# Kernel optimization log

Hardware: AMD Instinct MI355X
Metric: run time of the kernel (lower is better)

The kernel has to match this reference:

```python
import jax, jax.numpy as jnp
import numpy as np

D_MODEL = 1024
N_HEADS = 16
D_HEAD = D_MODEL // N_HEADS


def setup_inputs() -> dict:
    key = jax.random.key(0)
    ks = jax.random.split(key, 6)
    B, LQ, LK = 4, 512, 4096
    scale = 1.0 / np.sqrt(D_MODEL)
    return {
        "q_in": jax.random.normal(ks[0], (B, LQ, D_MODEL), dtype=jnp.float32),
        "mem": jax.random.normal(ks[1], (B, LK, D_MODEL), dtype=jnp.float32),
        "mem_mask": jnp.ones((B, 1, 1, LK), dtype=bool),
        "Wq": jax.random.normal(ks[2], (D_MODEL, D_MODEL), dtype=jnp.float32) * scale,
        "Wk": jax.random.normal(ks[3], (D_MODEL, D_MODEL), dtype=jnp.float32) * scale,
        "Wv": jax.random.normal(ks[4], (D_MODEL, D_MODEL), dtype=jnp.float32) * scale,
        "Wo": jax.random.normal(ks[5], (D_MODEL, D_MODEL), dtype=jnp.float32) * scale,
    }


def _split_heads(x):
    B, L, D = x.shape
    return x.reshape(B, L, N_HEADS, D_HEAD).transpose(0, 2, 1, 3)  # [B,H,L,Dh]


def reference(q_in, mem, mem_mask, Wq, Wk, Wv, Wo):
    # Linear layers use y = x @ W.T (torch nn.Linear convention, bias=False)
    q = _split_heads(q_in @ Wq.T)   # [B,H,Lq,Dh]
    k = _split_heads(mem @ Wk.T)    # [B,H,Lk,Dh]
    v = _split_heads(mem @ Wv.T)    # [B,H,Lk,Dh]
    scores = jnp.einsum('bhqd,bhkd->bhqk', q, k) / jnp.sqrt(jnp.float32(D_HEAD))
    scores = jnp.where(mem_mask, scores, -jnp.inf)
    attn = jax.nn.softmax(scores, axis=-1)  # dropout is identity at eval
    out = jnp.einsum('bhqk,bhkd->bhqd', attn, v)  # [B,H,Lq,Dh]
    B, H, LQ, Dh = out.shape
    out = out.transpose(0, 2, 1, 3).reshape(B, LQ, H * Dh)
    return out @ Wo.T
```

## Files before the change

kernel.cpp:

```cpp
#include <hip/hip_runtime.h>

#define D_MODEL 1024
#define NH 16
#define DH 64
#define BB 4
#define LQ 512
#define LK 4096

typedef __attribute__((ext_vector_type(8))) short bf16x8;
typedef __attribute__((ext_vector_type(4))) short bf16x4;
typedef __attribute__((ext_vector_type(4))) float f32x4;
typedef __attribute__((ext_vector_type(4))) unsigned short us4;

union U4 { unsigned int u[2]; bf16x4 v; };
union U8 { unsigned int u[4]; bf16x8 v; };

#define MFMA32(a, b, c) __builtin_amdgcn_mfma_f32_16x16x32_bf16(a, b, c, 0, 0, 0)

#if __has_builtin(__builtin_amdgcn_mfma_f32_16x16x16bf16_1k)
#define HAVE_MFMA16 1
#define MFMA16(a, b, c) __builtin_amdgcn_mfma_f32_16x16x16bf16_1k(a, b, c, 0, 0, 0)
#else
#define HAVE_MFMA16 0
#endif

#if __has_builtin(__builtin_amdgcn_exp2f)
#define EXP2F __builtin_amdgcn_exp2f
#else
__device__ __forceinline__ float EXP2F(float x) { return __expf(x * 0.69314718056f); }
#endif

#define PIPE_BAR(KEEP) asm volatile("s_waitcnt vmcnt(" #KEEP ") lgkmcnt(0)\n\ts_barrier" ::: "memory")
#define END_BAR()      asm volatile("s_waitcnt lgkmcnt(0)\n\ts_barrier" ::: "memory")

__device__ __forceinline__ unsigned short f2bf(float f) {
    unsigned int u = __float_as_uint(f);
    u += 0x7fffu + ((u >> 16) & 1u);
    return (unsigned short)(u >> 16);
}
__device__ __forceinline__ unsigned int packrn(float a, float b) {
    unsigned int ua = __float_as_uint(a) + 0x8000u;
    unsigned int ub = __float_as_uint(b) + 0x8000u;
    return __builtin_amdgcn_perm(ub, ua, 0x07060302u);
}
__device__ __forceinline__ void gld16(const void* g, void* l) {
    __builtin_amdgcn_global_load_lds(
        (__attribute__((address_space(1))) void*)(g),
        (__attribute__((address_space(3))) void*)(l), 16, 0, 0);
}
__device__ __forceinline__ unsigned int bperm(int srclane4, unsigned int v) {
    return (unsigned int)__builtin_amdgcn_ds_bpermute(srclane4, (int)v);
}

__global__ __launch_bounds__(256) void cvt_all(const float* __restrict__ q,
                                               const float* __restrict__ mem,
                                               const float* __restrict__ w0, const float* __restrict__ w1,
                                               const float* __restrict__ w2, const float* __restrict__ w3,
                                               unsigned short* __restrict__ dst) {
    constexpr size_t EQ = (size_t)BB * LQ * D_MODEL;
    constexpr size_t EM = (size_t)BB * LK * D_MODEL;
    constexpr size_t EW = (size_t)D_MODEL * D_MODEL;
    constexpr size_t R1 = EQ + EM;
    size_t i = ((size_t)blockIdx.x * 256 + threadIdx.x) * 4;
    const float* s; size_t o;
    if (i < EQ)                { s = q;   o = i; }
    else if (i < R1)           { s = mem; o = i - EQ; }
    else if (i < R1 + EW)      { s = w0;  o = i - R1; }
    else if (i < R1 + 2 * EW)  { s = w1;  o = i - R1 - EW; }
    else if (i < R1 + 3 * EW)  { s = w2;  o = i - R1 - 2 * EW; }
    else                       { s = w3;  o = i - R1 - 3 * EW; }
    float4 v = *(const float4*)(s + o);
    us4 ob;
    ob.x = f2bf(v.x); ob.y = f2bf(v.y); ob.z = f2bf(v.z); ob.w = f2bf(v.w);
    *(us4*)(dst + i) = ob;
}

#define GEMM_DECLS                                                                 \
    const int tid = threadIdx.x;                                                   \
    const int w = tid >> 6, lane = tid & 63;                                       \
    const int wr = (w >> 1) * 64, wc = (w & 1) * 64;                               \
    const int srow = lane >> 3, ssw = ((lane & 7) ^ srow) * 8;                     \
    const int fr = lane & 15, g = lane >> 4, frx = fr & 7;                         \
    f32x4 zero = {0.f, 0.f, 0.f, 0.f};                                             \
    f32x4 acc[4][4];                                                               \
    for (int i = 0; i < 4; ++i)                                                    \
        for (int j = 0; j < 4; ++j) acc[i][j] = zero;                              \
    const unsigned short* ga = A + (size_t)(m0 + w * 32 + srow) * 1024 + ssw;      \
    const unsigned short* gb = Bw + (size_t)(n0 + w * 32 + srow) * 1024 + ssw;

#define GEMM_ISSUE(PAR) do {                                                       \
    unsigned short* da = As + (PAR) * (128 * 64) + (w * 32) * 64;                  \
    unsigned short* db = Bs + (PAR) * (128 * 64) + (w * 32) * 64;                  \
    for (int c = 0; c < 4; ++c) {                                                  \
        gld16(ga + (size_t)c * 8 * 1024, da + c * 8 * 64);                         \
        gld16(gb + (size_t)c * 8 * 1024, db + c * 8 * 64);                         \
    }                                                                              \
    ga += 64; gb += 64;                                                            \
} while (0)

#define GEMM_COMPUTE(PAR) do {                                                     \
    const unsigned short* Ap = As + (PAR) * (128 * 64);                            \
    const unsigned short* Bp = Bs + (PAR) * (128 * 64);                            \
    for (int ks = 0; ks < 2; ++ks) {                                               \
        const int fx = ((ks * 4 + g) ^ frx) * 8;                                   \
        bf16x8 af[4], bfr[4];                                                      \
        for (int i = 0; i < 4; ++i) af[i] = *(const bf16x8*)(Ap + (wr + 16 * i + fr) * 64 + fx); \
        for (int j = 0; j < 4; ++j) bfr[j] = *(const bf16x8*)(Bp + (wc + 16 * j + fr) * 64 + fx); \
        for (int i = 0; i < 4; ++i)                                                \
            for (int j = 0; j < 4; ++j)                                            \
                acc[i][j] = MFMA32(af[i], bfr[j], acc[i][j]);                      \
    }                                                                              \
} while (0)

#define GEMM_PIPELINE                                                              \
    GEMM_ISSUE(0); GEMM_ISSUE(1);                                                  \
    for (int it = 0; it < 14; ++it) {                                              \
        PIPE_BAR(8);                                                               \
        GEMM_COMPUTE(it & 1);                                                      \
        END_BAR();                                                                 \
        GEMM_ISSUE(it & 1);                                                        \
    }                                                                              \
    PIPE_BAR(8);                                                                   \
    GEMM_COMPUTE(0);                                                               \
    PIPE_BAR(0);                                                                   \
    GEMM_COMPUTE(1);

#define SLOT_SH 8192

#define STAGE2(GB, LB, S, H) do {                                                  \
    const unsigned short* gs_ = (GB) + (size_t)(H) * 32;                           \
    unsigned short* ld_ = (LB) + (S) * SLOT_SH + tid * 8;                          \
    gld16(gs_, ld_);                                                               \
    gld16(gs_ + (size_t)131072, ld_ + 4096);          \
} while (0)

#define RD_A8(DST, SLOT) do {                                                      \
    const unsigned short* Ap_ = As + (size_t)(SLOT) * SLOT_SH + aoff;              \
    _Pragma("unroll")                                                              \
    for (int ii_ = 0; ii_ < 8; ++ii_)                                              \
        DST[ii_] = *(const bf16x8*)(Ap_ + ii_ * 512);                              \
} while (0)

#define RD_B(DST, SLOT) do {                                                       \
    const unsigned short* Bp_ = Bs + (size_t)(SLOT) * SLOT_SH + boff;              \
    _Pragma("unroll")                                                              \
    for (int jj_ = 0; jj_ < 4; ++jj_)                                              \
        DST[jj_] = *(const bf16x8*)(Bp_ + jj_ * 512);                              \
} while (0)

#define MM32(AF, BF) do {                                                          \
    __builtin_amdgcn_s_setprio(1);                                                 \
    _Pragma("unroll")                                                              \
    for (int ii = 0; ii < 8; ++ii) {                                               \
        _Pragma("unroll")                                                          \
        for (int jj = 0; jj < 4; ++jj)                                             \
            acc[ii][jj] = MFMA32(AF[ii], BF[jj], acc[ii][jj]);                     \
    }                                                                              \
    __builtin_amdgcn_s_setprio(0);                                                 \
} while (0)

#define VW(N)  asm volatile("s_waitcnt vmcnt(" #N ")" ::: "memory")
#define PEND() asm volatile("s_waitcnt lgkmcnt(0)\n\ts_barrier" ::: "memory")

#define WIN(H, AFC, BFC, AFN, BFN) do {                                            \
    const int sn_ = ((H) + 1) & 3;                                                 \
    RD_A8(AFN, sn_); RD_B(BFN, sn_);                                               \
    STAGE2(gA, As, ((H) + 3) & 3, (H) + 3);                                        \
    STAGE2(gB, Bs, ((H) + 3) & 3, (H) + 3);                                        \
    MM32(AFC, BFC);                                                                \
    VW(4);                                                                         \
    PEND();                                                                        \
} while (0)

__global__ __launch_bounds__(512, 2) void proj256(const unsigned short* __restrict__ memb,
                                                  const unsigned short* __restrict__ W,
                                                  unsigned short* __restrict__ Kp,
                                                  unsigned short* __restrict__ Vt) {
    __shared__ alignas(16) unsigned short As[4 * SLOT_SH];
    __shared__ alignas(16) unsigned short Bs[4 * SLOT_SH];
    const int x = blockIdx.x;
    const int xcd = x & 7, s = x >> 3;
    const int rnd = s >> 5, i5 = s & 31;
    const int mt = xcd * 8 + rnd * 4 + (i5 >> 3);
    const int strip = i5 & 7;
    const int isV = strip >> 2, nt = strip & 3;
    const int m0 = mt * 256, n0 = nt * 256;
    const unsigned short* Bw = W + ((size_t)(1 + isV) << 20);

    const int tid = threadIdx.x;
    const int lane = tid & 63, wid = tid >> 6;
    const int wm = wid >> 2, wn = wid & 3;
    const int fr = lane & 15, g = lane >> 4;
    const int sfr = (fr >> 1) & 3;
    const int aoff = (wm * 128 + fr) * 32 + ((g ^ sfr) << 3);
    const int boff = (wn * 64 + fr) * 32 + ((g ^ sfr) << 3);

    f32x4 zero = {0.f, 0.f, 0.f, 0.f};
    f32x4 acc[8][4];
#pragma unroll
    for (int i = 0; i < 8; ++i)
#pragma unroll
        for (int j = 0; j < 4; ++j) acc[i][j] = zero;

    const int srow = tid >> 2;
    const int scg = (tid & 3) ^ ((tid >> 3) & 3);
    const unsigned short* gA = memb + (size_t)(m0 + srow) * 1024 + scg * 8;
    const unsigned short* gB = Bw + (size_t)(n0 + srow) * 1024 + scg * 8;

    bf16x8 afA[8], afB[8], bfA[4], bfB[4];

    STAGE2(gA, As, 0, 0); STAGE2(gB, Bs, 0, 0);
    STAGE2(gA, As, 1, 1); STAGE2(gB, Bs, 1, 1);
    STAGE2(gA, As, 2, 2); STAGE2(gB, Bs, 2, 2);
    VW(4);
    asm volatile("s_barrier" ::: "memory");
    RD_A8(afA, 0); RD_B(bfA, 0);

    for (int u = 0; u < 14; ++u) {
        WIN(2 * u,     afA, bfA, afB, bfB);
        WIN(2 * u + 1, afB, bfB, afA, bfA);
    }
    WIN(28, afA, bfA, afB, bfB);
    RD_A8(afA, 2); RD_B(bfA, 2);
    MM32(afB, bfB);
    VW(0);
    PEND();
    RD_A8(afB, 3); RD_B(bfB, 3);
    MM32(afA, bfA);
    PEND();
    MM32(afB, bfB);

    const int cl = fr;
    if (!isV) {
#pragma unroll
        for (int i = 0; i < 8; ++i)
#pragma unroll
            for (int j = 0; j < 4; ++j)
#pragma unroll
                for (int r = 0; r < 4; ++r) {
                    int m = m0 + wm * 128 + 16 * i + g * 4 + r;
                    int n = n0 + wn * 64 + 16 * j + cl;
                    Kp[(size_t)m * 1024 + n] = f2bf(acc[i][j][r]);
                }
    } else {
#pragma unroll
        for (int i = 0; i < 8; ++i)
#pragma unroll
            for (int j = 0; j < 4; ++j) {
                int m = m0 + wm * 128 + 16 * i + g * 4;
                int n = n0 + wn * 64 + 16 * j + cl;
                int b = m >> 12, tt2 = m & 4095;
                int h = n >> 6, d = n & 63;
                us4 ov;
                ov.x = f2bf(acc[i][j][0]); ov.y = f2bf(acc[i][j][1]);
                ov.z = f2bf(acc[i][j][2]); ov.w = f2bf(acc[i][j][3]);
                *(us4*)(Vt + ((size_t)(b * NH + h) * DH + d) * LK + tt2) = ov;
            }
    }
}

__global__ __launch_bounds__(256, 2) void proj_q(const unsigned short* __restrict__ qb,
                                                 const unsigned short* __restrict__ W,
                                                 unsigned short* __restrict__ Qp) {
    __shared__ alignas(16) unsigned short As[2 * 128 * 64];
    __shared__ alignas(16) unsigned short Bs[2 * 128 * 64];
    const int x = blockIdx.x;
    const int mt = x & 15, nt = x >> 4;
    const unsigned short* A = qb;
    const unsigned short* Bw = W;
    const int m0 = mt * 128, n0 = nt * 128;

    GEMM_DECLS
    GEMM_PIPELINE

    const int cl = lane & 15;
    const float QSCALE = 0.18033688011112042f;
    for (int i = 0; i < 4; ++i)
        for (int j = 0; j < 4; ++j)
            for (int r = 0; r < 4; ++r) {
                int m = m0 + wr + 16 * i + g * 4 + r;
                int n = n0 + wc + 16 * j + cl;
                Qp[(size_t)m * 1024 + n] = f2bf(acc[i][j][r] * QSCALE);
            }
}

__global__ __launch_bounds__(256, 2) void gemm_o(const unsigned short* __restrict__ A,
                                                 const unsigned short* __restrict__ Bw,
                                                 float* __restrict__ C) {
    __shared__ alignas(16) unsigned short As[2 * 128 * 64];
    __shared__ alignas(16) unsigned short Bs[2 * 128 * 64];
    const int m0 = blockIdx.x * 128, n0 = blockIdx.y * 128;

    GEMM_DECLS
    GEMM_PIPELINE

    const int cl = lane & 15;
    for (int i = 0; i < 4; ++i)
        for (int j = 0; j < 4; ++j)
            for (int r = 0; r < 4; ++r) {
                int m = m0 + wr + 16 * i + g * 4 + r;
                int n = n0 + wc + 16 * j + cl;
                C[(size_t)m * 1024 + n] = acc[i][j][r];
            }
}

__global__ __launch_bounds__(256, 4) void attn(const unsigned short* __restrict__ Qp,
                                               const unsigned short* __restrict__ Kp,
                                               const unsigned short* __restrict__ Vt,
                                               float* __restrict__ OP, float* __restrict__ Lp) {
    __shared__ alignas(16) unsigned short Ks[2 * 64 * 64];
    __shared__ alignas(16) unsigned short Vs[2 * 64 * 64];
    const int tid = threadIdx.x, w = tid >> 6, lane = tid & 63;
    const int gid = blockIdx.x, qt = blockIdx.y;
    const int h = gid & 15, bck = gid >> 4;
    const int b = bck >> 2, ck = bck & 3;
    const int cl = lane & 15, g = lane >> 4;
    const int rx = cl & 7;

    bf16x8 bq[2][2];
    for (int cg = 0; cg < 2; ++cg) {
        const size_t qrow = (size_t)(b * LQ + qt * 128 + w * 32 + cg * 16 + cl) * D_MODEL + h * DH;
        bq[cg][0] = *(const bf16x8*)(Qp + qrow + g * 8);
        bq[cg][1] = *(const bf16x8*)(Qp + qrow + 32 + g * 8);
    }

    float l_run[2] = {0.f, 0.f};
    f32x4 zero = {0.f, 0.f, 0.f, 0.f};
    f32x4 o[2][4];
    for (int cg = 0; cg < 2; ++cg)
        for (int i = 0; i < 4; ++i) o[cg][i] = zero;

    const int srow = lane >> 3;
    const int ssw = ((lane & 7) ^ srow) * 8;
    const int k0 = ck * (LK / 4);
    const unsigned short* kp = Kp + (size_t)b * LK * D_MODEL + h * DH +
                               (size_t)(k0 + w * 16 + srow) * D_MODEL + ssw;
    const unsigned short* vp = Vt + (size_t)(b * NH + h) * DH * LK +
                               (size_t)(w * 16 + srow) * LK + k0 + ssw;

#define ATTN_ISSUE(PAR) do {                                                   \
    unsigned short* kd = Ks + (PAR) * (64 * 64) + (w * 16) * 64;               \
    unsigned short* vd = Vs + (PAR) * (64 * 64) + (w * 16) * 64;               \
    gld16(kp, kd); gld16(kp + (size_t)8 * D_MODEL, kd + 8 * 64);               \
    gld16(vp, vd); gld16(vp + (size_t)8 * LK, vd + 8 * 64);                    \
    kp += (size_t)64 * D_MODEL; vp += 64;                                      \
} while (0)

#if HAVE_MFMA16
#define ATTN_PV(PAR) do {                                                      \
    for (int md = 0; md < 4; ++md) {                                           \
        const unsigned short* vr = Vs + (PAR) * (64 * 64) + (md * 16 + cl) * 64; \
        for (int ksv = 0; ksv < 4; ++ksv) {                                    \
            bf16x4 av = *(const bf16x4*)(vr + (((2 * ksv + (g >> 1)) ^ rx) << 3) + ((g & 1) << 2)); \
            for (int cg = 0; cg < 2; ++cg) {                                   \
                U4 pb; pb.u[0] = pk0[cg][ksv]; pb.u[1] = pk1[cg][ksv];         \
                o[cg][md] = MFMA16(av, pb.v, o[cg][md]);                       \
            }                                                                  \
        }                                                                      \
    }                                                                          \
} while (0)
#else
#define ATTN_PV(PAR) do {                                                      \
    for (int cg = 0; cg < 2; ++cg) {                                           \
        const int selA = ((((g & 1) << 5) | cl)) << 2;                         \
        const int selB = selA + 64;                                            \
        const int hi = g >> 1;                                                 \
        unsigned int ax0 = bperm(selA, pk0[cg][0]), ax1 = bperm(selA, pk0[cg][1]); \
        unsigned int ay0 = bperm(selA, pk1[cg][0]), ay1 = bperm(selA, pk1[cg][1]); \
        unsigned int bx0 = bperm(selB, pk0[cg][0]), bx1 = bperm(selB, pk0[cg][1]); \
        unsigned int by0 = bperm(selB, pk1[cg][0]), by1 = bperm(selB, pk1[cg][1]); \
        U8 b0;                                                                 \
        b0.u[0] = hi ? ax1 : ax0; b0.u[1] = hi ? ay1 : ay0;                    \
        b0.u[2] = hi ? bx1 : bx0; b0.u[3] = hi ? by1 : by0;                    \
        unsigned int cx0 = bperm(selA, pk0[cg][2]), cx1 = bperm(selA, pk0[cg][3]); \
        unsigned int cy0 = bperm(selA, pk1[cg][2]), cy1 = bperm(selA, pk1[cg][3]); \
        unsigned int dx0 = bperm(selB, pk0[cg][2]), dx1 = bperm(selB, pk0[cg][3]); \
        unsigned int dy0 = bperm(selB, pk1[cg][2]), dy1 = bperm(selB, pk1[cg][3]); \
        U8 b1;                                                                 \
        b1.u[0] = hi ? cx1 : cx0; b1.u[1] = hi ? cy1 : cy0;                    \
        b1.u[2] = hi ? dx1 : dx0; b1.u[3] = hi ? dy1 : dy0;                    \
        for (int md = 0; md < 4; ++md) {                                       \
            const unsigned short* vr = Vs + (PAR) * (64 * 64) + (md * 16 + cl) * 64; \
            bf16x8 av0 = *(const bf16x8*)(vr + ((g ^ rx) << 3));               \
            bf16x8 av1 = *(const bf16x8*)(vr + (((4 + g) ^ rx) << 3));         \
            o[cg][md] = MFMA32(av0, b0.v, o[cg][md]);                          \
            o[cg][md] = MFMA32(av1, b1.v, o[cg][md]);                          \
        }                                                                      \
    }                                                                          \
} while (0)
#endif

#define ATTN_COMPUTE(PAR) do {                                                 \
    unsigned int pk0[2][4], pk1[2][4];                                         \
    for (int mt = 0; mt < 4; ++mt) {                                           \
        const unsigned short* kr = Ks + (PAR) * (64 * 64) + (mt * 16 + cl) * 64; \
        bf16x8 a0 = *(const bf16x8*)(kr + ((g ^ rx) << 3));                    \
        bf16x8 a1 = *(const bf16x8*)(kr + (((4 + g) ^ rx) << 3));              \
        for (int cg = 0; cg < 2; ++cg) {                                       \
            f32x4 z = zero;                                                    \
            z = MFMA32(a0, bq[cg][0], z);                                      \
            z = MFMA32(a1, bq[cg][1], z);                                      \
            float p0 = EXP2F(z[0]), p1 = EXP2F(z[1]);                          \
            float p2 = EXP2F(z[2]), p3 = EXP2F(z[3]);                          \
            l_run[cg] += (p0 + p1) + (p2 + p3);                                \
            pk0[cg][mt] = packrn(p0, p1);                                      \
            pk1[cg][mt] = packrn(p2, p3);                                      \
        }                                                                      \
    }                                                                          \
    ATTN_PV(PAR);                                                              \
} while (0)

    ATTN_ISSUE(0); ATTN_ISSUE(1);
    for (int it = 0; it < 14; ++it) {
        PIPE_BAR(4);
        ATTN_COMPUTE(it & 1);
        END_BAR();
        ATTN_ISSUE(it & 1);
    }
    PIPE_BAR(4);
    ATTN_COMPUTE(0);
    PIPE_BAR(0);
    ATTN_COMPUTE(1);

    for (int cg = 0; cg < 2; ++cg) {
        float l = l_run[cg];
        l += __shfl_xor(l, 16);
        l += __shfl_xor(l, 32);
        const int q = qt * 128 + w * 32 + cg * 16 + cl;
        const size_t pidx = ((size_t)(b * NH + h) * LQ + q) * 4 + ck;
        for (int md = 0; md < 4; ++md)
            *(f32x4*)(OP + pidx * 64 + md * 16 + g * 4) = o[cg][md];
        if (g == 0) Lp[pidx] = l;
    }
}

__global__ __launch_bounds__(256) void combine(const float* __restrict__ OP,
                                               const float* __restrict__ Lp,
                                               unsigned short* __restrict__ AO) {
    int t = blockIdx.x * 256 + threadIdx.x;
    int bhq = t >> 4, dg = (t & 15) * 4;
    float4 L4 = *(const float4*)(Lp + (size_t)bhq * 4);
    float inv = 1.f / (((L4.x + L4.y) + (L4.z + L4.w)));
    float4 acc = make_float4(0.f, 0.f, 0.f, 0.f);
    for (int c = 0; c < 4; ++c) {
        float4 v = *(const float4*)(OP + (size_t)(bhq * 4 + c) * 64 + dg);
        acc.x += v.x; acc.y += v.y; acc.z += v.z; acc.w += v.w;
    }
    int b = bhq >> 13, h = (bhq >> 9) & 15, q = bhq & 511;
    us4 ob;
    ob.x = f2bf(acc.x * inv); ob.y = f2bf(acc.y * inv);
    ob.z = f2bf(acc.z * inv); ob.w = f2bf(acc.w * inv);
    *(us4*)(AO + (size_t)(b * LQ + q) * D_MODEL + h * DH + dg) = ob;
}

extern "C" void kernel_launch(void* const* d_in, const int* in_sizes, int n_in,
                              void* d_out, int out_size, void* d_ws, size_t ws_size,
                              hipStream_t stream) {
    const float* q_in = (const float*)d_in[0];
    const float* mem  = (const float*)d_in[1];
    const float* Wq = (const float*)d_in[3];
    const float* Wk = (const float*)d_in[4];
    const float* Wv = (const float*)d_in[5];
    const float* Wo = (const float*)d_in[6];
    float* out = (float*)d_out;

    constexpr size_t E_Q = (size_t)BB * LQ * D_MODEL;
    constexpr size_t E_M = (size_t)BB * LK * D_MODEL;
    constexpr size_t E_W = (size_t)D_MODEL * D_MODEL;
    constexpr size_t E_OP = (size_t)BB * NH * LQ * 4 * 64;
    constexpr size_t E_L  = (size_t)BB * NH * LQ * 4;

    float* OP = (float*)d_ws;
    float* Lp = OP + E_OP;
    unsigned short* qb   = (unsigned short*)(Lp + E_L);
    unsigned short* memb = qb + E_Q;
    unsigned short* wqb  = memb + E_M;
    unsigned short* wob  = wqb + 3 * E_W;
    unsigned short* Qp   = wob + E_W;
    unsigned short* Kp   = Qp + E_Q;
    unsigned short* Vt   = Kp + E_M;
    unsigned short* AO   = Vt + E_M;

    constexpr int CVT_BLK = (int)((E_Q + E_M + 4 * E_W) / 4 / 256);
    cvt_all<<<CVT_BLK, 256, 0, stream>>>(q_in, mem, Wq, Wk, Wv, Wo, qb);

    proj256<<<512, 512, 0, stream>>>(memb, wqb, Kp, Vt);
    proj_q<<<128, 256, 0, stream>>>(qb, wqb, Qp);

    attn<<<dim3(256, 4), 256, 0, stream>>>(Qp, Kp, Vt, OP, Lp);
    combine<<<2048, 256, 0, stream>>>(OP, Lp, AO);

    gemm_o<<<dim3(16, 8), 256, 0, stream>>>(AO, wob, out);
}
```

Before: 281.2 us.

## Load B-operand fragments directly from global memory, bypassing LDS staging

In the K/V projection GEMM, the weight (B) operand is now read by each wave straight from global memory into registers, one iteration ahead. It is no longer staged through a 4-slot LDS ring. This halves LDS usage and removes the B-side LDS writes and reads. The cost is uncoalesced, redundant global loads of weight rows across waves, with global latency now sitting on the critical path, and retuned vmcnt waits whose correctness depends on how loads are counted.

```diff
diff --git a/kernel.cpp b/kernel.cpp
--- a/kernel.cpp
+++ b/kernel.cpp
@@ -141,11 +141,10 @@
         DST[ii_] = *(const bf16x8*)(Ap_ + ii_ * 512);                              \
 } while (0)
 
-#define RD_B(DST, SLOT) do {                                                       \
-    const unsigned short* Bp_ = Bs + (size_t)(SLOT) * SLOT_SH + boff;              \
+#define LOADB(DST, H) do {                                                         \
     _Pragma("unroll")                                                              \
     for (int jj_ = 0; jj_ < 4; ++jj_)                                              \
-        DST[jj_] = *(const bf16x8*)(Bp_ + jj_ * 512);                              \
+        DST[jj_] = *(const bf16x8*)(gBB + (size_t)jj_ * 16 * 1024 + (size_t)(H) * 32); \
 } while (0)
 
 #define MM32(AF, BF) do {                                                          \
@@ -163,12 +162,11 @@
 #define PEND() asm volatile("s_waitcnt lgkmcnt(0)\n\ts_barrier" ::: "memory")
 
 #define WIN(H, AFC, BFC, AFN, BFN) do {                                            \
-    const int sn_ = ((H) + 1) & 3;                                                 \
-    RD_A8(AFN, sn_); RD_B(BFN, sn_);                                               \
+    RD_A8(AFN, ((H) + 1) & 3);                                                     \
     STAGE2(gA, As, ((H) + 3) & 3, (H) + 3);                                        \
-    STAGE2(gB, Bs, ((H) + 3) & 3, (H) + 3);                                        \
+    LOADB(BFN, (H) + 1);                                                           \
     MM32(AFC, BFC);                                                                \
-    VW(4);                                                                         \
+    VW(6);                                                                         \
     PEND();                                                                        \
 } while (0)
 
@@ -177,7 +175,6 @@
                                                   unsigned short* __restrict__ Kp,
                                                   unsigned short* __restrict__ Vt) {
     __shared__ alignas(16) unsigned short As[4 * SLOT_SH];
-    __shared__ alignas(16) unsigned short Bs[4 * SLOT_SH];
     const int x = blockIdx.x;
     const int xcd = x & 7, s = x >> 3;
     const int rnd = s >> 5, i5 = s & 31;
@@ -193,7 +190,8 @@
     const int fr = lane & 15, g = lane >> 4;
     const int sfr = (fr >> 1) & 3;
     const int aoff = (wm * 128 + fr) * 32 + ((g ^ sfr) << 3);
-    const int boff = (wn * 64 + fr) * 32 + ((g ^ sfr) << 3);
+
+    const unsigned short* gBB = Bw + (size_t)(n0 + wn * 64 + fr) * 1024 + g * 8;
 
     f32x4 zero = {0.f, 0.f, 0.f, 0.f};
     f32x4 acc[8][4];
@@ -205,30 +203,35 @@
     const int srow = tid >> 2;
     const int scg = (tid & 3) ^ ((tid >> 3) & 3);
     const unsigned short* gA = memb + (size_t)(m0 + srow) * 1024 + scg * 8;
-    const unsigned short* gB = Bw + (size_t)(n0 + srow) * 1024 + scg * 8;
-
-    bf16x8 afA[8], afB[8], bfA[4], bfB[4];
-
-    STAGE2(gA, As, 0, 0); STAGE2(gB, Bs, 0, 0);
-    STAGE2(gA, As, 1, 1); STAGE2(gB, Bs, 1, 1);
-    STAGE2(gA, As, 2, 2); STAGE2(gB, Bs, 2, 2);
+
+    bf16x8 afA[8], afB[8], bBA[4], bBB[4];
+
+    STAGE2(gA, As, 0, 0);
+    STAGE2(gA, As, 1, 1);
+    STAGE2(gA, As, 2, 2);
+    LOADB(bBA, 0);
+    VW(0);
+    asm volatile("s_barrier" ::: "memory");
+    RD_A8(afA, 0);
+
+    for (int u = 0; u < 7; ++u) {
+        WIN(4 * u,     afA, bBA, afB, bBB);
+        WIN(4 * u + 1, afB, bBB, afA, bBA);
+        WIN(4 * u + 2, afA, bBA, afB, bBB);
+        WIN(4 * u + 3, afB, bBB, afA, bBA);
+    }
+    WIN(28, afA, bBA, afB, bBB);
+    RD_A8(afA, 2);
+    LOADB(bBA, 30);
+    MM32(afB, bBB);
     VW(4);
-    asm volatile("s_barrier" ::: "memory");
-    RD_A8(afA, 0); RD_B(bfA, 0);
-
-    for (int u = 0; u < 14; ++u) {
-        WIN(2 * u,     afA, bfA, afB, bfB);
-        WIN(2 * u + 1, afB, bfB, afA, bfA);
-    }
-    WIN(28, afA, bfA, afB, bfB);
-    RD_A8(afA, 2); RD_B(bfA, 2);
-    MM32(afB, bfB);
-    VW(0);
     PEND();
-    RD_A8(afB, 3); RD_B(bfB, 3);
-    MM32(afA, bfA);
+    RD_A8(afB, 3);
+    LOADB(bBB, 31);
+    MM32(afA, bBA);
+    VW(4);
     PEND();
-    MM32(afB, bfB);
+    MM32(afB, bBB);
 
     const int cl = fr;
     if (!isV) {
```

Measured after the change: 320.2 us. +13.9%, slower.
